# Performance work log

Hardware: AMD Instinct MI355X
Metric: run time of the kernel (lower is better)

The kernel has to match this reference:

```python
import jax, jax.numpy as jnp
import numpy as np

W_GLOBAL, W_SOFT, W_HARD = 0.2, 0.3, 0.5
GAMMA, ALPHA = 2.0, 0.25
MIN_TEMP, MAX_TEMP = 0.01, 100.0
EPS = 1e-12


def _l2norm(x, axis):
    n = jnp.sqrt(jnp.sum(x * x, axis=axis, keepdims=True))
    return x / jnp.maximum(n, EPS)


def _focal_ce(logits, labels):
    # torch F.cross_entropy with label_smoothing=ALPHA, then focal modulation
    log_p = jax.nn.log_softmax(logits, axis=-1)           # (B, K)
    nll = -jnp.take_along_axis(log_p, labels[:, None], axis=-1)[:, 0]
    smooth = -jnp.mean(log_p, axis=-1)
    ce = (1.0 - ALPHA) * nll + ALPHA * smooth
    pt = jnp.exp(-ce)
    return jnp.mean((1.0 - pt) ** GAMMA * ce)


def setup_inputs() -> dict:
    key = jax.random.key(0)
    k1, k2, k3 = jax.random.split(key, 3)
    B, C, N = 256, 512, 512
    yolo_feats = jax.random.normal(k1, (B, C, N), dtype=jnp.float32)
    clip_feats = jax.random.normal(k2, (B, C), dtype=jnp.float32)
    logit_scale = jax.random.uniform(k3, (1,), dtype=jnp.float32) * 2.0 + 2.0
    return {"yolo_feats": yolo_feats, "clip_feats": clip_feats, "logit_scale": logit_scale}


def reference(yolo_feats, clip_feats, logit_scale):
    yolo_feats = _l2norm(yolo_feats, axis=1)              # (B, C, N)
    clip_feats = _l2norm(clip_feats, axis=1)              # (B, C)
    scale = jnp.clip(jnp.exp(logit_scale), MIN_TEMP, MAX_TEMP)  # (1,)
    B = yolo_feats.shape[0]
    labels = jnp.arange(B, dtype=jnp.int32)

    # global branch
    yolo_global = _l2norm(jnp.mean(yolo_feats, axis=2), axis=1)   # (B, C)
    sim_global = (yolo_global @ clip_feats.T) * scale             # (B, B)
    loss_global = 0.5 * (_focal_ce(sim_global, labels) + _focal_ce(sim_global.T, labels))

    # dense spatial similarity map (B, N, K=B)
    sim_map = jnp.einsum('bcn,kc->bnk', yolo_feats, clip_feats) * scale

    sim_soft = jax.nn.logsumexp(sim_map, axis=1)                  # (B, B)
    loss_soft = 0.5 * (_focal_ce(sim_soft, labels) + _focal_ce(sim_soft.T, labels))

    sim_hard = jnp.max(sim_map, axis=1)                           # (B, B)
    loss_hard = 0.5 * (_focal_ce(sim_hard, labels) + _focal_ce(sim_hard.T, labels))

    return W_GLOBAL * loss_global + W_SOFT * loss_soft + W_HARD * loss_hard
```

## Files before the change

kernel.cpp:

```cpp
#include <hip/hip_runtime.h>
#include <math.h>

constexpr int B = 256;
constexpr int C = 512;
constexpr int N = 512;
constexpr int K = 256;

constexpr size_t OFF_CLIPNB = 0;
constexpr size_t OFF_INV    = OFF_CLIPNB + (size_t)B*C/2;
constexpr size_t OFF_SGLOB  = OFF_INV   + (size_t)B*N;
constexpr size_t OFF_SSOFT  = OFF_SGLOB + (size_t)B*K;
constexpr size_t OFF_SHARD  = OFF_SSOFT + (size_t)B*K;
constexpr size_t OFF_PM     = OFF_SHARD + (size_t)B*K;
constexpr size_t OFF_PS     = OFF_PM    + (size_t)2*B*K;
constexpr size_t OFF_PH     = OFF_PS    + (size_t)2*B*K;
constexpr size_t OFF_PG     = OFF_PH    + (size_t)2*B*K;
constexpr size_t OFF_GN     = OFF_PG    + (size_t)2*B*K;
constexpr size_t OFF_MISC   = OFF_GN    + (size_t)B;

typedef __attribute__((ext_vector_type(8))) short short8;
typedef __attribute__((ext_vector_type(4))) float f32x4;

__device__ __forceinline__ float wave_reduce_sum(float v) {
  #pragma unroll
  for (int off = 32; off > 0; off >>= 1) v += __shfl_xor(v, off, 64);
  return v;
}
__device__ __forceinline__ float wave_reduce_max(float v) {
  #pragma unroll
  for (int off = 32; off > 0; off >>= 1) v = fmaxf(v, __shfl_xor(v, off, 64));
  return v;
}
__device__ __forceinline__ unsigned int bf16_rne(float x) {
  unsigned int u = __builtin_bit_cast(unsigned int, x);
  return (u + 0x7FFFu + ((u >> 16) & 1u)) >> 16;
}
__device__ __forceinline__ unsigned int pk_bf16(float x, float y) {
  return bf16_rne(x) | (bf16_rne(y) << 16);
}

__global__ void k_misc(const float* __restrict__ ls, float* __restrict__ misc) {
  int t = threadIdx.x;
  if (t == 0) misc[0] = fminf(fmaxf(expf(ls[0]), 0.01f), 100.0f);
  if (t >= 1 && t < 7) misc[t] = 0.0f;
}

__global__ __launch_bounds__(256) void k_rownorm(const float* __restrict__ src,
                                                 unsigned short* __restrict__ dst_bf) {
  int b = blockIdx.x, t = threadIdx.x;
  float x0 = src[(size_t)b * C + t];
  float x1 = src[(size_t)b * C + t + 256];
  __shared__ float red[4];
  float w = wave_reduce_sum(x0 * x0 + x1 * x1);
  if ((t & 63) == 0) red[t >> 6] = w;
  __syncthreads();
  float tot = red[0] + red[1] + red[2] + red[3];
  float r = 1.0f / fmaxf(sqrtf(tot), 1e-12f);
  dst_bf[(size_t)b * C + t] = (unsigned short)bf16_rne(x0 * r);
  dst_bf[(size_t)b * C + t + 256] = (unsigned short)bf16_rne(x1 * r);
}

__global__ __launch_bounds__(256, 2) void k_main_mfma(
    const float* __restrict__ yolo,
    const unsigned short* __restrict__ clipnb,
    const float* __restrict__ misc,
    float* __restrict__ invg,
    float* __restrict__ PM, float* __restrict__ PS, float* __restrict__ PH,
    float* __restrict__ PG) {
  int bh = blockIdx.x;
  int b = bh >> 1, half = bh & 1;
  int t = threadIdx.x;
  int w = t >> 6, lane = t & 63;
  int quad = lane >> 4, col = lane & 15;

  __shared__ unsigned int xl[128 * 32];
  __shared__ float ssqb[8 * 128];
  __shared__ float invt[128];

  const float scale = misc[0];
  const float* ybase = yolo + (size_t)b * C * N;

  int nf = t & 31;
  int cp0 = t >> 5;
  unsigned int rotv = (8u * (nf & 3) + 4u * (unsigned)(nf >> 2)) & 31u;

  float msk[16], ssk[16], hsk[16];
  #pragma unroll
  for (int i = 0; i < 16; i++) { msk[i] = -1e30f; ssk[i] = 0.f; hsk[i] = -1e30f; }

  for (int iter = 0; iter < 2; iter++) {
    int n0 = half * 256 + iter * 128;
    float4 ssq4 = {0.f, 0.f, 0.f, 0.f};

    f32x4 acc[4][8];
    #pragma unroll
    for (int kt = 0; kt < 4; kt++)
      #pragma unroll
      for (int nt = 0; nt < 8; nt++) {
        f32x4 z = {0.f, 0.f, 0.f, 0.f};
        acc[kt][nt] = z;
      }

    for (int cc = 0; cc < 8; cc++) {
      int c0 = cc * 64;
      __syncthreads();

      short8 afr[4][2];
      #pragma unroll
      for (int kt = 0; kt < 4; kt++)
        #pragma unroll
        for (int s = 0; s < 2; s++) {
          const unsigned short* ap =
              clipnb + (size_t)(64 * w + 16 * kt + col) * C + c0 + 32 * s + 8 * quad;
          union { uint4 u; short8 v; } fa;
          fa.u = *(const uint4*)ap;
          afr[kt][s] = fa.v;
        }

      #pragma unroll
      for (int p = 0; p < 4; p++) {
        int cp = cp0 + 8 * p;
        int c = c0 + 2 * cp;
        const float* pa = ybase + (size_t)c * N + n0 + 4 * nf;
        float4 a = *(const float4*)pa;
        float4 bb = *(const float4*)(pa + N);
        ssq4.x += a.x * a.x + bb.x * bb.x;
        ssq4.y += a.y * a.y + bb.y * bb.y;
        ssq4.z += a.z * a.z + bb.z * bb.z;
        ssq4.w += a.w * a.w + bb.w * bb.w;
        unsigned int pos = ((unsigned)cp + rotv) & 31u;
        int base0 = (4 * nf) * 32;
        xl[base0 + pos]       = pk_bf16(a.x, bb.x);
        xl[base0 + 32 + pos]  = pk_bf16(a.y, bb.y);
        xl[base0 + 64 + pos]  = pk_bf16(a.z, bb.z);
        xl[base0 + 96 + pos]  = pk_bf16(a.w, bb.w);
      }
      __syncthreads();

      #pragma unroll
      for (int s = 0; s < 2; s++) {
        #pragma unroll
        for (int nt = 0; nt < 8; nt++) {
          int n = 16 * nt + col;
          unsigned int pos =
              (unsigned)(16 * s + 4 * quad + 8 * (col >> 2) + 4 * nt) & 31u;
          union { uint4 u; short8 v; } fb;
          fb.u = *(const uint4*)&xl[n * 32 + pos];
          #pragma unroll
          for (int kt = 0; kt < 4; kt++)
            acc[kt][nt] = __builtin_amdgcn_mfma_f32_16x16x32_bf16(
                afr[kt][s], fb.v, acc[kt][nt], 0, 0, 0);
        }
      }
    }

    {
      int base = cp0 * 128 + 4 * nf;
      ssqb[base + 0] = ssq4.x;
      ssqb[base + 1] = ssq4.y;
      ssqb[base + 2] = ssq4.z;
      ssqb[base + 3] = ssq4.w;
    }
    __syncthreads();
    if (t < 128) {
      float s = 0.f;
      #pragma unroll
      for (int g = 0; g < 8; g++) s += ssqb[g * 128 + t];
      float iv = 1.0f / fmaxf(sqrtf(s), 1e-12f);
      invt[t] = iv;
      invg[(size_t)b * N + n0 + t] = iv;
    }
    __syncthreads();

    float invn[8];
    #pragma unroll
    for (int nt = 0; nt < 8; nt++) invn[nt] = invt[16 * nt + col];
    #pragma unroll
    for (int kt = 0; kt < 4; kt++)
      #pragma unroll
      for (int r = 0; r < 4; r++) {
        int idx = kt * 4 + r;
        float mm = msk[idx], ss = ssk[idx], hh = hsk[idx], gg = 0.f;
        #pragma unroll
        for (int nt = 0; nt < 8; nt++) {
          float vu = acc[kt][nt][r] * invn[nt];
          gg += vu;
          float v = vu * scale;
          hh = fmaxf(hh, v);
          float M = fmaxf(mm, v);
          ss = ss * __expf(mm - M) + __expf(v - M);
          mm = M;
        }
        msk[idx] = mm; ssk[idx] = ss; hsk[idx] = hh;
        #pragma unroll
        for (int o = 1; o < 16; o <<= 1) gg += __shfl_xor(gg, o, 64);
        if (col == 0) {
          size_t a = (size_t)bh * 256 + (64 * w + 16 * kt + 4 * quad + r);
          if (iter == 0) PG[a] = gg; else PG[a] += gg;
        }
      }
  }

  #pragma unroll
  for (int idx = 0; idx < 16; idx++) {
    float mm = msk[idx], ss = ssk[idx], hh = hsk[idx];
    #pragma unroll
    for (int o = 1; o < 16; o <<= 1) {
      float mo = __shfl_xor(mm, o, 64);
      float so = __shfl_xor(ss, o, 64);
      float ho = __shfl_xor(hh, o, 64);
      float M = fmaxf(mm, mo);
      ss = ss * __expf(mm - M) + so * __expf(mo - M);
      mm = M;
      hh = fmaxf(hh, ho);
    }
    msk[idx] = mm; ssk[idx] = ss; hsk[idx] = hh;
  }
  if (col == 0) {
    size_t pbase = (size_t)bh * 256;
    #pragma unroll
    for (int kt = 0; kt < 4; kt++)
      #pragma unroll
      for (int r = 0; r < 4; r++) {
        int k = 64 * w + 16 * kt + 4 * quad + r;
        int idx = kt * 4 + r;
        PM[pbase + k] = msk[idx];
        PS[pbase + k] = ssk[idx];
        PH[pbase + k] = hsk[idx];
      }
  }
}

__global__ __launch_bounds__(512) void k_gnorm(const float* __restrict__ yolo,
                                               const float* __restrict__ invg,
                                               float* __restrict__ gn) {
  int b = blockIdx.x;
  int t = threadIdx.x;
  int w = t >> 6, lane = t & 63;
  const float* xb = yolo + (size_t)b * C * N;
  const float* ivb = invg + (size_t)b * N;
  float4 iv[2];
  #pragma unroll
  for (int p = 0; p < 2; p++) iv[p] = *(const float4*)(ivb + p * 256 + 4 * lane);
  float sq = 0.f;
  for (int ci = 0; ci < 64; ci++) {
    int c = w * 64 + ci;
    const float* row = xb + (size_t)c * N + 4 * lane;
    float cs = 0.f;
    #pragma unroll
    for (int p = 0; p < 2; p++) {
      float4 v = *(const float4*)(row + p * 256);
      cs += v.x * iv[p].x + v.y * iv[p].y + v.z * iv[p].z + v.w * iv[p].w;
    }
    cs = wave_reduce_sum(cs);
    sq += cs * cs;
  }
  __shared__ float red[8];
  if (lane == 0) red[w] = sq;
  __syncthreads();
  if (t == 0) {
    float s = 0.f;
    #pragma unroll
    for (int g = 0; g < 8; g++) s += red[g];
    gn[b] = fmaxf(sqrtf(s) * (1.0f / (float)N), 1e-12f);
  }
}

__global__ __launch_bounds__(256) void k_sglob(const float* __restrict__ PG,
                                               const float* __restrict__ gn,
                                               const float* __restrict__ misc,
                                               float* __restrict__ Sglob) {
  int i = blockIdx.x, k = threadIdx.x;
  float v = PG[(size_t)(2 * i) * 256 + k] + PG[(size_t)(2 * i + 1) * 256 + k];
  Sglob[(size_t)i * K + k] = misc[0] * v * (1.0f / (float)N) / gn[i];
}

__global__ __launch_bounds__(256) void k_merge(const float* __restrict__ PM,
                                               const float* __restrict__ PS,
                                               const float* __restrict__ PH,
                                               float* __restrict__ Ssoft,
                                               float* __restrict__ Shard) {
  int b = blockIdx.x, k = threadIdx.x;
  size_t p0 = (size_t)(2 * b) * 256 + k;
  size_t p1 = (size_t)(2 * b + 1) * 256 + k;
  float m0 = PM[p0], m1 = PM[p1];
  float M = fmaxf(m0, m1);
  float S = PS[p0] * __expf(m0 - M) + PS[p1] * __expf(m1 - M);
  Ssoft[(size_t)b * K + k] = M + __logf(S);
  Shard[(size_t)b * K + k] = fmaxf(PH[p0], PH[p1]);
}

__global__ __launch_bounds__(256) void k_focal(const float* __restrict__ Sglob,
                                               const float* __restrict__ Ssoft,
                                               const float* __restrict__ Shard,
                                               float* __restrict__ misc) {
  int job = blockIdx.y;
  int i = blockIdx.x;
  int t = threadIdx.x;
  const float* M = job < 2 ? Sglob : (job < 4 ? Ssoft : Shard);
  float v = (job & 1) ? M[(size_t)t * K + i] : M[(size_t)i * K + t];
  __shared__ float red[4];
  float mx = wave_reduce_max(v);
  if ((t & 63) == 0) red[t >> 6] = mx;
  __syncthreads();
  mx = fmaxf(fmaxf(red[0], red[1]), fmaxf(red[2], red[3]));
  __syncthreads();
  float sv = wave_reduce_sum(v);
  if ((t & 63) == 0) red[t >> 6] = sv;
  __syncthreads();
  float sumv = red[0] + red[1] + red[2] + red[3];
  __syncthreads();
  float se = wave_reduce_sum(expf(v - mx));
  if ((t & 63) == 0) red[t >> 6] = se;
  __syncthreads();
  if (t == 0) {
    float sumexp = red[0] + red[1] + red[2] + red[3];
    float logZ = mx + logf(sumexp);
    float diag = M[(size_t)i * K + i];
    float nll = logZ - diag;
    float smooth = logZ - sumv * (1.0f / 256.0f);
    float ce = 0.75f * nll + 0.25f * smooth;
    float pt = expf(-ce);
    float fo = (1.0f - pt) * (1.0f - pt) * ce;
    atomicAdd(&misc[1 + job], fo);
  }
}

__global__ void k_finish(const float* __restrict__ misc, float* __restrict__ out) {
  float lg = misc[1] + misc[2];
  float ls = misc[3] + misc[4];
  float lh = misc[5] + misc[6];
  out[0] = (0.2f * lg + 0.3f * ls + 0.5f * lh) * 0.5f * (1.0f / 256.0f);
}

extern "C" void kernel_launch(void* const* d_in, const int* in_sizes, int n_in,
                              void* d_out, int out_size, void* d_ws, size_t ws_size,
                              hipStream_t stream) {
  const float* yolo = (const float*)d_in[0];
  const float* clip = (const float*)d_in[1];
  const float* ls   = (const float*)d_in[2];
  float* out = (float*)d_out;
  float* ws = (float*)d_ws;
  unsigned short* clipnb = (unsigned short*)(ws + OFF_CLIPNB);
  float* invg  = ws + OFF_INV;
  float* Sglob = ws + OFF_SGLOB;
  float* Ssoft = ws + OFF_SSOFT;
  float* Shard = ws + OFF_SHARD;
  float* PM    = ws + OFF_PM;
  float* PS    = ws + OFF_PS;
  float* PH    = ws + OFF_PH;
  float* PG    = ws + OFF_PG;
  float* gn    = ws + OFF_GN;
  float* misc  = ws + OFF_MISC;

  k_misc<<<1, 64, 0, stream>>>(ls, misc);
  k_rownorm<<<256, 256, 0, stream>>>(clip, clipnb);
  k_main_mfma<<<512, 256, 0, stream>>>(yolo, clipnb, misc, invg, PM, PS, PH, PG);
  k_gnorm<<<256, 512, 0, stream>>>(yolo, invg, gn);
  k_sglob<<<256, 256, 0, stream>>>(PG, gn, misc, Sglob);
  k_merge<<<256, 256, 0, stream>>>(PM, PS, PH, Ssoft, Shard);
  k_focal<<<dim3(256, 6), 256, 0, stream>>>(Sglob, Ssoft, Shard, misc);
  k_finish<<<1, 1, 0, stream>>>(misc, out);
}
```

Baseline: 475.6 us.

## Precompute column norms, double-buffer LDS with register prefetch, fuse global-mean and merge passes

Adds a separate pass that computes the per-pixel inverse norms first. The main MFMA kernel can then normalize yolo features before the bf16 conversion and accumulate per-channel sums for the global branch in the same pass, which removes the second full read of yolo that k_gnorm did. The main loop now double-buffers LDS and prefetches the next chunk's yolo values into registers, so one barrier per chunk is enough and loads overlap MFMA work. Partial softmax, max and sum statistics are written per 128-column slot and merged in one post kernel that replaces k_gnorm, k_sglob and k_merge. The cost is an extra full read of yolo in k_inv, more shuffle reductions, and higher register and LDS use.

Measured after the change: 537.7 us. 1.13x slower.

```diff
diff --git a/kernel.cpp b/kernel.cpp
--- a/kernel.cpp
+++ b/kernel.cpp
@@ -8,15 +8,15 @@
 
 constexpr size_t OFF_CLIPNB = 0;
 constexpr size_t OFF_INV    = OFF_CLIPNB + (size_t)B*C/2;
-constexpr size_t OFF_SGLOB  = OFF_INV   + (size_t)B*N;
-constexpr size_t OFF_SSOFT  = OFF_SGLOB + (size_t)B*K;
-constexpr size_t OFF_SHARD  = OFF_SSOFT + (size_t)B*K;
-constexpr size_t OFF_PM     = OFF_SHARD + (size_t)B*K;
-constexpr size_t OFF_PS     = OFF_PM    + (size_t)2*B*K;
-constexpr size_t OFF_PH     = OFF_PS    + (size_t)2*B*K;
-constexpr size_t OFF_PG     = OFF_PH    + (size_t)2*B*K;
-constexpr size_t OFF_GN     = OFF_PG    + (size_t)2*B*K;
-constexpr size_t OFF_MISC   = OFF_GN    + (size_t)B;
+constexpr size_t OFF_U4     = OFF_INV    + (size_t)B*N;
+constexpr size_t OFF_PM     = OFF_U4     + (size_t)1024*C;
+constexpr size_t OFF_PS     = OFF_PM     + (size_t)1024*K;
+constexpr size_t OFF_PH     = OFF_PS     + (size_t)1024*K;
+constexpr size_t OFF_PG     = OFF_PH     + (size_t)1024*K;
+constexpr size_t OFF_SGLOB  = OFF_PG     + (size_t)1024*K;
+constexpr size_t OFF_SSOFT  = OFF_SGLOB  + (size_t)B*K;
+constexpr size_t OFF_SHARD  = OFF_SSOFT  + (size_t)B*K;
+constexpr size_t OFF_MISC   = OFF_SHARD  + (size_t)B*K;
 
 typedef __attribute__((ext_vector_type(8))) short short8;
 typedef __attribute__((ext_vector_type(4))) float f32x4;
@@ -60,22 +60,46 @@
   dst_bf[(size_t)b * C + t + 256] = (unsigned short)bf16_rne(x1 * r);
 }
 
+__global__ __launch_bounds__(512) void k_inv(const float* __restrict__ yolo,
+                                             float* __restrict__ invg) {
+  int bh = blockIdx.x;
+  int b = bh >> 1, half = bh & 1;
+  int t = threadIdx.x;
+  int slice = t >> 6, lane = t & 63;
+  const float* base = yolo + (size_t)b * C * N + half * 256 + 4 * lane;
+  float4 ss = {0.f, 0.f, 0.f, 0.f};
+  #pragma unroll 8
+  for (int ci = 0; ci < 64; ci++) {
+    float4 v = *(const float4*)(base + (size_t)(slice * 64 + ci) * N);
+    ss.x += v.x * v.x; ss.y += v.y * v.y;
+    ss.z += v.z * v.z; ss.w += v.w * v.w;
+  }
+  __shared__ float part[8][256];
+  *(float4*)&part[slice][4 * lane] = ss;
+  __syncthreads();
+  if (t < 256) {
+    float s = 0.f;
+    #pragma unroll
+    for (int g = 0; g < 8; g++) s += part[g][t];
+    invg[(size_t)b * N + half * 256 + t] = 1.0f / fmaxf(sqrtf(s), 1e-12f);
+  }
+}
+
 __global__ __launch_bounds__(256, 2) void k_main_mfma(
     const float* __restrict__ yolo,
     const unsigned short* __restrict__ clipnb,
+    const float* __restrict__ invg,
     const float* __restrict__ misc,
-    float* __restrict__ invg,
-    float* __restrict__ PM, float* __restrict__ PS, float* __restrict__ PH,
-    float* __restrict__ PG) {
+    float* __restrict__ U4,
+    float* __restrict__ PM2, float* __restrict__ PS2,
+    float* __restrict__ PH2, float* __restrict__ PG2) {
   int bh = blockIdx.x;
   int b = bh >> 1, half = bh & 1;
   int t = threadIdx.x;
   int w = t >> 6, lane = t & 63;
   int quad = lane >> 4, col = lane & 15;
 
-  __shared__ unsigned int xl[128 * 32];
-  __shared__ float ssqb[8 * 128];
-  __shared__ float invt[128];
+  __shared__ unsigned int xl[2][128 * 32];
 
   const float scale = misc[0];
   const float* ybase = yolo + (size_t)b * C * N;
@@ -84,13 +108,10 @@
   int cp0 = t >> 5;
   unsigned int rotv = (8u * (nf & 3) + 4u * (unsigned)(nf >> 2)) & 31u;
 
-  float msk[16], ssk[16], hsk[16];
-  #pragma unroll
-  for (int i = 0; i < 16; i++) { msk[i] = -1e30f; ssk[i] = 0.f; hsk[i] = -1e30f; }
-
+  #pragma unroll 1
   for (int iter = 0; iter < 2; iter++) {
     int n0 = half * 256 + iter * 128;
-    float4 ssq4 = {0.f, 0.f, 0.f, 0.f};
+    float4 iv4 = *(const float4*)(invg + (size_t)b * N + n0 + 4 * nf);
 
     f32x4 acc[4][8];
     #pragma unroll
@@ -101,10 +122,45 @@
         acc[kt][nt] = z;
       }
 
+    float4 Ya[4], Yb[4];
+    #pragma unroll
+    for (int p = 0; p < 4; p++) {
+      const float* pa = ybase + (size_t)(2 * (cp0 + 8 * p)) * N + n0 + 4 * nf;
+      Ya[p] = *(const float4*)pa;
+      Yb[p] = *(const float4*)(pa + N);
+    }
+
+    #pragma unroll
     for (int cc = 0; cc < 8; cc++) {
+      unsigned int* xbuf = &xl[cc & 1][0];
       int c0 = cc * 64;
-      __syncthreads();
-
+
+      float up[8];
+      #pragma unroll
+      for (int p = 0; p < 4; p++) {
+        float ax = Ya[p].x * iv4.x, ay = Ya[p].y * iv4.y,
+              az = Ya[p].z * iv4.z, aw = Ya[p].w * iv4.w;
+        float bx = Yb[p].x * iv4.x, by = Yb[p].y * iv4.y,
+              bz = Yb[p].z * iv4.z, bw = Yb[p].w * iv4.w;
+        unsigned int pos = ((unsigned)(cp0 + 8 * p) + rotv) & 31u;
+        int base0 = (4 * nf) * 32;
+        xbuf[base0 + pos]       = pk_bf16(ax, bx);
+        xbuf[base0 + 32 + pos]  = pk_bf16(ay, by);
+        xbuf[base0 + 64 + pos]  = pk_bf16(az, bz);
+        xbuf[base0 + 96 + pos]  = pk_bf16(aw, bw);
+        up[2 * p]     = ax + ay + az + aw;
+        up[2 * p + 1] = bx + by + bz + bw;
+      }
+
+      if (cc < 7) {
+        #pragma unroll
+        for (int p = 0; p < 4; p++) {
+          const float* pa =
+              ybase + (size_t)((cc + 1) * 64 + 2 * (cp0 + 8 * p)) * N + n0 + 4 * nf;
+          Ya[p] = *(const float4*)pa;
+          Yb[p] = *(const float4*)(pa + N);
+        }
+      }
       short8 afr[4][2];
       #pragma unroll
       for (int kt = 0; kt < 4; kt++)
@@ -118,24 +174,21 @@
         }
 
       #pragma unroll
-      for (int p = 0; p < 4; p++) {
-        int cp = cp0 + 8 * p;
-        int c = c0 + 2 * cp;
-        const float* pa = ybase + (size_t)c * N + n0 + 4 * nf;
-        float4 a = *(const float4*)pa;
-        float4 bb = *(const float4*)(pa + N);
-        ssq4.x += a.x * a.x + bb.x * bb.x;
-        ssq4.y += a.y * a.y + bb.y * bb.y;
-        ssq4.z += a.z * a.z + bb.z * bb.z;
-        ssq4.w += a.w * a.w + bb.w * bb.w;
-        unsigned int pos = ((unsigned)cp + rotv) & 31u;
-        int base0 = (4 * nf) * 32;
-        xl[base0 + pos]       = pk_bf16(a.x, bb.x);
-        xl[base0 + 32 + pos]  = pk_bf16(a.y, bb.y);
-        xl[base0 + 64 + pos]  = pk_bf16(a.z, bb.z);
-        xl[base0 + 96 + pos]  = pk_bf16(a.w, bb.w);
-      }
-      __syncthreads();
+      for (int i = 0; i < 8; i++)
+        #pragma unroll
+        for (int o = 1; o < 32; o <<= 1)
+          up[i] += __shfl_xor(up[i], o, 64);
+      if (nf == 0) {
+        size_t ub = ((size_t)bh * 2 + iter) * C;
+        #pragma unroll
+        for (int p = 0; p < 4; p++) {
+          int c = c0 + 2 * (cp0 + 8 * p);
+          *(float2*)&U4[ub + c] = make_float2(up[2 * p], up[2 * p + 1]);
+        }
+      }
+
+      asm volatile("s_waitcnt lgkmcnt(0)" ::: "memory");
+      __builtin_amdgcn_s_barrier();
 
       #pragma unroll
       for (int s = 0; s < 2; s++) {
@@ -145,7 +198,7 @@
           unsigned int pos =
               (unsigned)(16 * s + 4 * quad + 8 * (col >> 2) + 4 * nt) & 31u;
           union { uint4 u; short8 v; } fb;
-          fb.u = *(const uint4*)&xl[n * 32 + pos];
+          fb.u = *(const uint4*)&xbuf[n * 32 + pos];
           #pragma unroll
           for (int kt = 0; kt < 4; kt++)
             acc[kt][nt] = __builtin_amdgcn_mfma_f32_16x16x32_bf16(
@@ -154,36 +207,15 @@
       }
     }
 
-    {
-      int base = cp0 * 128 + 4 * nf;
-      ssqb[base + 0] = ssq4.x;
-      ssqb[base + 1] = ssq4.y;
-      ssqb[base + 2] = ssq4.z;
-      ssqb[base + 3] = ssq4.w;
-    }
-    __syncthreads();
-    if (t < 128) {
-      float s = 0.f;
-      #pragma unroll
-      for (int g = 0; g < 8; g++) s += ssqb[g * 128 + t];
-      float iv = 1.0f / fmaxf(sqrtf(s), 1e-12f);
-      invt[t] = iv;
-      invg[(size_t)b * N + n0 + t] = iv;
-    }
-    __syncthreads();
-
-    float invn[8];
-    #pragma unroll
-    for (int nt = 0; nt < 8; nt++) invn[nt] = invt[16 * nt + col];
+    size_t slot = (size_t)bh * 2 + iter;
     #pragma unroll
     for (int kt = 0; kt < 4; kt++)
       #pragma unroll
       for (int r = 0; r < 4; r++) {
-        int idx = kt * 4 + r;
-        float mm = msk[idx], ss = ssk[idx], hh = hsk[idx], gg = 0.f;
+        float mm = -1e30f, ss = 0.f, hh = -1e30f, gg = 0.f;
         #pragma unroll
         for (int nt = 0; nt < 8; nt++) {
-          float vu = acc[kt][nt][r] * invn[nt];
+          float vu = acc[kt][nt][r];
           gg += vu;
           float v = vu * scale;
           hh = fmaxf(hh, v);
@@ -191,103 +223,64 @@
           ss = ss * __expf(mm - M) + __expf(v - M);
           mm = M;
         }
-        msk[idx] = mm; ssk[idx] = ss; hsk[idx] = hh;
-        #pragma unroll
-        for (int o = 1; o < 16; o <<= 1) gg += __shfl_xor(gg, o, 64);
+        #pragma unroll
+        for (int o = 1; o < 16; o <<= 1) {
+          float mo = __shfl_xor(mm, o, 64);
+          float so = __shfl_xor(ss, o, 64);
+          float ho = __shfl_xor(hh, o, 64);
+          float go = __shfl_xor(gg, o, 64);
+          float M = fmaxf(mm, mo);
+          ss = ss * __expf(mm - M) + so * __expf(mo - M);
+          mm = M;
+          hh = fmaxf(hh, ho);
+          gg += go;
+        }
         if (col == 0) {
-          size_t a = (size_t)bh * 256 + (64 * w + 16 * kt + 4 * quad + r);
-          if (iter == 0) PG[a] = gg; else PG[a] += gg;
-        }
-      }
-  }
-
+          int k = 64 * w + 16 * kt + 4 * quad + r;
+          size_t a = slot * 256 + k;
+          PM2[a] = mm; PS2[a] = ss; PH2[a] = hh; PG2[a] = gg;
+        }
+      }
+  }
+}
+
+__global__ __launch_bounds__(256) void k_post(
+    const float* __restrict__ U4, const float* __restrict__ PG2,
+    const float* __restrict__ PM2, const float* __restrict__ PS2,
+    const float* __restrict__ PH2, const float* __restrict__ misc,
+    float* __restrict__ Sglob, float* __restrict__ Ssoft,
+    float* __restrict__ Shard) {
+  int bI = blockIdx.x;
+  int t = threadIdx.x;
+  __shared__ float red[4];
+  __shared__ float gnS;
+  float sq = 0.f;
   #pragma unroll
-  for (int idx = 0; idx < 16; idx++) {
-    float mm = msk[idx], ss = ssk[idx], hh = hsk[idx];
-    #pragma unroll
-    for (int o = 1; o < 16; o <<= 1) {
-      float mo = __shfl_xor(mm, o, 64);
-      float so = __shfl_xor(ss, o, 64);
-      float ho = __shfl_xor(hh, o, 64);
-      float M = fmaxf(mm, mo);
-      ss = ss * __expf(mm - M) + so * __expf(mo - M);
-      mm = M;
-      hh = fmaxf(hh, ho);
-    }
-    msk[idx] = mm; ssk[idx] = ss; hsk[idx] = hh;
-  }
-  if (col == 0) {
-    size_t pbase = (size_t)bh * 256;
-    #pragma unroll
-    for (int kt = 0; kt < 4; kt++)
-      #pragma unroll
-      for (int r = 0; r < 4; r++) {
-        int k = 64 * w + 16 * kt + 4 * quad + r;
-        int idx = kt * 4 + r;
-        PM[pbase + k] = msk[idx];
-        PS[pbase + k] = ssk[idx];
-        PH[pbase + k] = hsk[idx];
-      }
-  }
-}
-
-__global__ __launch_bounds__(512) void k_gnorm(const float* __restrict__ yolo,
-                                               const float* __restrict__ invg,
-                                               float* __restrict__ gn) {
-  int b = blockIdx.x;
-  int t = threadIdx.x;
-  int w = t >> 6, lane = t & 63;
-  const float* xb = yolo + (size_t)b * C * N;
-  const float* ivb = invg + (size_t)b * N;
-  float4 iv[2];
-  #pragma unroll
-  for (int p = 0; p < 2; p++) iv[p] = *(const float4*)(ivb + p * 256 + 4 * lane);
-  float sq = 0.f;
-  for (int ci = 0; ci < 64; ci++) {
-    int c = w * 64 + ci;
-    const float* row = xb + (size_t)c * N + 4 * lane;
-    float cs = 0.f;
-    #pragma unroll
-    for (int p = 0; p < 2; p++) {
-      float4 v = *(const float4*)(row + p * 256);
-      cs += v.x * iv[p].x + v.y * iv[p].y + v.z * iv[p].z + v.w * iv[p].w;
-    }
-    cs = wave_reduce_sum(cs);
-    sq += cs * cs;
-  }
-  __shared__ float red[8];
-  if (lane == 0) red[w] = sq;
+  for (int cq = 0; cq < 2; cq++) {
+    size_t u0 = ((size_t)bI * 4) * C + t + 256 * cq;
+    float tot = U4[u0] + U4[u0 + C] + U4[u0 + 2 * C] + U4[u0 + 3 * C];
+    sq += tot * tot;
+  }
+  float wsum = wave_reduce_sum(sq);
+  if ((t & 63) == 0) red[t >> 6] = wsum;
   __syncthreads();
   if (t == 0) {
-    float s = 0.f;
-    #pragma unroll
-    for (int g = 0; g < 8; g++) s += red[g];
-    gn[b] = fmaxf(sqrtf(s) * (1.0f / (float)N), 1e-12f);
-  }
-}
-
-__global__ __launch_bounds__(256) void k_sglob(const float* __restrict__ PG,
-                                               const float* __restrict__ gn,
-                                               const float* __restrict__ misc,
-                                               float* __restrict__ Sglob) {
-  int i = blockIdx.x, k = threadIdx.x;
-  float v = PG[(size_t)(2 * i) * 256 + k] + PG[(size_t)(2 * i + 1) * 256 + k];
-  Sglob[(size_t)i * K + k] = misc[0] * v * (1.0f / (float)N) / gn[i];
-}
-
-__global__ __launch_bounds__(256) void k_merge(const float* __restrict__ PM,
-                                               const float* __restrict__ PS,
-                                               const float* __restrict__ PH,
-                                               float* __restrict__ Ssoft,
-                                               float* __restrict__ Shard) {
-  int b = blockIdx.x, k = threadIdx.x;
-  size_t p0 = (size_t)(2 * b) * 256 + k;
-  size_t p1 = (size_t)(2 * b + 1) * 256 + k;
-  float m0 = PM[p0], m1 = PM[p1];
-  float M = fmaxf(m0, m1);
-  float S = PS[p0] * __expf(m0 - M) + PS[p1] * __expf(m1 - M);
-  Ssoft[(size_t)b * K + k] = M + __logf(S);
-  Shard[(size_t)b * K + k] = fmaxf(PH[p0], PH[p1]);
+    float s = red[0] + red[1] + red[2] + red[3];
+    gnS = fmaxf(sqrtf(s) * (1.0f / (float)N), 1e-12f);
+  }
+  __syncthreads();
+  float gn = gnS;
+  int k = t;
+  size_t p0 = (size_t)bI * 4 * 256 + k;
+  float g = PG2[p0] + PG2[p0 + 256] + PG2[p0 + 512] + PG2[p0 + 768];
+  Sglob[(size_t)bI * K + k] = misc[0] * g * (1.0f / (float)N) / gn;
+  float m0 = PM2[p0], m1 = PM2[p0 + 256], m2 = PM2[p0 + 512], m3 = PM2[p0 + 768];
+  float M = fmaxf(fmaxf(m0, m1), fmaxf(m2, m3));
+  float S = PS2[p0] * __expf(m0 - M) + PS2[p0 + 256] * __expf(m1 - M) +
+            PS2[p0 + 512] * __expf(m2 - M) + PS2[p0 + 768] * __expf(m3 - M);
+  Ssoft[(size_t)bI * K + k] = M + __logf(S);
+  Shard[(size_t)bI * K + k] =
+      fmaxf(fmaxf(PH2[p0], PH2[p0 + 256]), fmaxf(PH2[p0 + 512], PH2[p0 + 768]));
 }
 
 __global__ __launch_bounds__(256) void k_focal(const float* __restrict__ Sglob,
@@ -343,22 +336,23 @@
   float* ws = (float*)d_ws;
   unsigned short* clipnb = (unsigned short*)(ws + OFF_CLIPNB);
   float* invg  = ws + OFF_INV;
+  float* U4    = ws + OFF_U4;
+  float* PM2   = ws + OFF_PM;
+  float* PS2   = ws + OFF_PS;
+  float* PH2   = ws + OFF_PH;
+  float* PG2   = ws + OFF_PG;
   float* Sglob = ws + OFF_SGLOB;
   float* Ssoft = ws + OFF_SSOFT;
   float* Shard = ws + OFF_SHARD;
-  float* PM    = ws + OFF_PM;
-  float* PS    = ws + OFF_PS;
-  float* PH    = ws + OFF_PH;
-  float* PG    = ws + OFF_PG;
-  float* gn    = ws + OFF_GN;
   float* misc  = ws + OFF_MISC;
 
   k_misc<<<1, 64, 0, stream>>>(ls, misc);
   k_rownorm<<<256, 256, 0, stream>>>(clip, clipnb);
-  k_main_mfma<<<512, 256, 0, stream>>>(yolo, clipnb, misc, invg, PM, PS, PH, PG);
-  k_gnorm<<<256, 512, 0, stream>>>(yolo, invg, gn);
-  k_sglob<<<256, 256, 0, stream>>>(PG, gn, misc, Sglob);
-  k_merge<<<256, 256, 0, stream>>>(PM, PS, PH, Ssoft, Shard);
+  k_inv<<<512, 512, 0, stream>>>(yolo, invg);
+  k_main_mfma<<<512, 256, 0, stream>>>(yolo, clipnb, invg, misc, U4,
+                                       PM2, PS2, PH2, PG2);
+  k_post<<<256, 256, 0, stream>>>(U4, PG2, PM2, PS2, PH2, misc,
+                                  Sglob, Ssoft, Shard);
   k_focal<<<dim3(256, 6), 256, 0, stream>>>(Sglob, Ssoft, Shard, misc);
   k_finish<<<1, 1, 0, stream>>>(misc, out);
 }
```
